# Kernel optimization log

Measured on AMD Instinct MI355X. Metric: run time of the kernel, lower is better.

The kernel has to match this reference:

```python
import jax, jax.numpy as jnp
import numpy as np

B, N, K = 8, 2048, 20  # clouds, points per cloud, knn


def _lin(k, i, o):
    kw, kb = jax.random.split(k)
    w = jax.random.normal(kw, (i, o), jnp.float32) / np.sqrt(i)
    b = jax.random.normal(kb, (o,), jnp.float32) * 0.01
    return w, b


def setup_inputs():
    key = jax.random.key(0)
    ks = jax.random.split(key, 9)
    pos = jax.random.normal(ks[0], (B * N, 3), jnp.float32)
    w11, b11 = _lin(ks[1], 3, 64)
    w12, b12 = _lin(ks[2], 64, 64)
    w13, b13 = _lin(ks[3], 64, 64)
    w21, b21 = _lin(ks[4], 192, 128)
    wh1, bh1 = _lin(ks[5], 128, 1024)
    wh2, bh2 = _lin(ks[6], 1024, 512)
    wh3, bh3 = _lin(ks[7], 512, 265)
    wh4, bh4 = _lin(ks[8], 265, 40)
    o, z = jnp.ones, jnp.zeros
    return dict(
        pos=pos,
        w11=w11, b11=b11, g11=o(64), be11=z(64),
        w12=w12, b12=b12, g12=o(64), be12=z(64),
        w13=w13, b13=b13, g13=o(64), be13=z(64),
        w21=w21, b21=b21, g21=o(128), be21=z(128),
        wh1=wh1, bh1=bh1, gh1=o(1024), beh1=z(1024),
        wh2=wh2, bh2=bh2, gh2=o(512), beh2=z(512),
        wh3=wh3, bh3=bh3, gh3=o(265), beh3=z(265),
        wh4=wh4, bh4=bh4,
    )


def _bn(x, g, b):
    # BatchNorm1d in training mode: stats over all leading dims, biased var.
    ax = tuple(range(x.ndim - 1))
    m = x.mean(ax)
    v = x.var(ax)
    return (x - m) * jax.lax.rsqrt(v + 1e-5) * g + b


def _forward(pos, w11, b11, g11, be11, w12, b12, g12, be12, w13, b13, g13, be13,
             w21, b21, g21, be21, wh1, bh1, gh1, beh1, wh2, bh2, gh2, beh2,
             wh3, bh3, gh3, beh3, wh4, bh4):
    p = pos.reshape(B, N, 3)
    # knn_graph per cloud, loop=False
    d2 = jnp.sum(p * p, -1)                                   # [B,N]
    dist = d2[:, :, None] + d2[:, None, :] - 2.0 * jnp.einsum('bnd,bmd->bnm', p, p)
    dist = dist + jnp.eye(N, dtype=pos.dtype) * 1e10          # exclude self
    _, idx = jax.lax.top_k(-dist, K)                          # [B,N,K]
    nb = jax.vmap(lambda a, i: a[i])(p, idx)                  # [B,N,K,3]
    rel = nb - p[:, :, None, :]                               # relative neighbor offsets
    # local PCA frame per point (V_t)
    cov = jnp.einsum('bnkd,bnke->bnde', rel, rel)             # [B,N,3,3]
    _, V = jnp.linalg.eigh(cov)                               # columns = principal dirs
    loc = jnp.einsum('bnkd,bnde->bnke', rel, V)               # rel pos in local frame
    # DD1: edge MLP (conv_p) + directional max pool (out_3d)
    h = _bn(jax.nn.relu(loc @ w11 + b11), g11, be11)
    h = _bn(jax.nn.relu(h @ w12 + b12), g12, be12)
    h = _bn(jax.nn.relu(h @ w13 + b13), g13, be13)            # [B,N,K,64]
    f3d = jnp.max(h[..., None] * loc[..., None, :], axis=2)   # [B,N,64,3]
    # DD2: gather neighbor 3d features (conv_fn), rotate into center frame, MLP, max pool
    fj = jax.vmap(lambda a, i: a[i])(f3d, idx)                # [B,N,K,64,3]
    fj_loc = jnp.einsum('bnkcd,bnde->bnkce', fj, V)
    h2 = _bn(jax.nn.relu(fj_loc.reshape(B, N, K, 192) @ w21 + b21), g21, be21)
    fdd2 = jnp.max(h2, axis=2).reshape(B * N, 128)
    # head
    y1 = (fdd2 @ wh1 + bh1).reshape(B, N, 1024).max(axis=1)
    y1 = _bn(jax.nn.relu(y1), gh1, beh1)
    y2 = _bn(jax.nn.relu(y1 @ wh2 + bh2), gh2, beh2)
    y3 = _bn(jax.nn.relu(y2 @ wh3 + bh3), gh3, beh3)
    return jax.nn.log_softmax(y3 @ wh4 + bh4, axis=1)         # [B,40]


def reference(pos, w11, b11, g11, be11, w12, b12, g12, be12, w13, b13, g13, be13,
              w21, b21, g21, be21, wh1, bh1, gh1, beh1, wh2, bh2, gh2, beh2,
              wh3, bh3, gh3, beh3, wh4, bh4):
    return _forward(pos, w11, b11, g11, be11, w12, b12, g12, be12, w13, b13, g13, be13,
                    w21, b21, g21, be21, wh1, bh1, gh1, beh1, wh2, bh2, gh2, beh2,
                    wh3, bh3, gh3, beh3, wh4, bh4)
```

## Files before the change

### kernel.cpp

```cpp
#include <hip/hip_runtime.h>


#define NEW_SLARTG 1

typedef unsigned short u16;
typedef unsigned int u32;
typedef unsigned long long u64;
typedef __attribute__((ext_vector_type(8))) short short8;
typedef __attribute__((ext_vector_type(4))) float f32x4;

#define BB 8
#define NNp 2048
#define KKn 20
#define NP 16384
#define EE 327680

__device__ __forceinline__ u32 fkey(float f) {
  u32 u = __float_as_uint(f);
  return (u & 0x80000000u) ? ~u : (u | 0x80000000u);
}
__device__ __forceinline__ float funkey(u32 k) {
  u32 u = (k & 0x80000000u) ? (k ^ 0x80000000u) : ~k;
  return __uint_as_float(u);
}
__device__ __forceinline__ float f_sign(float a, float b) {
  return (b >= 0.f) ? fabsf(a) : -fabsf(a);
}
__device__ __forceinline__ u16 f2bf(float f) {
  u32 u = __float_as_uint(f);
  u32 r = (u + 0x7fffu + ((u >> 16) & 1u)) >> 16;
  return (u16)r;
}

__device__ __forceinline__ u64 sxor64(u64 v, int m) {
  union { u64 q; u32 d[2]; } a; a.q = v;
  a.d[0] = __shfl_xor(a.d[0], m);
  a.d[1] = __shfl_xor(a.d[1], m);
  return a.q;
}
__device__ __forceinline__ u64 sidx64(u64 v, int src) {
  union { u64 q; u32 d[2]; } a; a.q = v;
  a.d[0] = __shfl(a.d[0], src);
  a.d[1] = __shfl(a.d[1], src);
  return a.q;
}
__device__ __forceinline__ void bsort64(u64& v, int lane) {
#pragma unroll
  for (int k = 2; k <= 64; k <<= 1) {
#pragma unroll
    for (int j = k >> 1; j > 0; j >>= 1) {
      u64 pv = sxor64(v, j);
      bool up = ((lane & k) == 0);
      bool lower = ((lane & j) == 0);
      bool keepmin = (lower == up);
      bool take = keepmin ? (pv < v) : (pv > v);
      v = take ? pv : v;
    }
  }
}

__device__ float slapy2_(float x, float y) {
#pragma clang fp contract(off)
  float xa = fabsf(x), ya = fabsf(y);
  float w = fmaxf(xa, ya), z = fminf(xa, ya);
  if (z == 0.f) return w;
  float t = z / w;
  return w * sqrtf(1.0f + t * t);
}

__device__ void slartg_(float f, float g, float& c, float& s, float& r) {
#pragma clang fp contract(off)
#if NEW_SLARTG
  const float safmin = 1.17549435e-38f;
  const float safmax = 8.50705917e+37f;
  const float rtmin = 1.08420217e-19f;
  const float rtmax = 6.52221171e+18f;
  float f1 = fabsf(f), g1 = fabsf(g);
  if (g == 0.f) { c = 1.f; s = 0.f; r = f; }
  else if (f == 0.f) { c = 0.f; s = (g >= 0.f) ? 1.f : -1.f; r = g1; }
  else {
    float d;
    if (f1 > rtmin && f1 < rtmax && g1 > rtmin && g1 < rtmax) {
      d = sqrtf(f * f + g * g);
      c = f1 / d;
      r = (f >= 0.f) ? d : -d;
    } else {
      float uu = fminf(safmax, fmaxf(safmin, fmaxf(f1, g1)));
      float fs = f / uu, gs = g / uu;
      d = sqrtf(fs * fs + gs * gs);
      c = fabsf(fs) / d;
      r = ((f >= 0.f) ? d : -d) * uu;
    }
    s = g / r;
  }
#else
  if (g == 0.f) { c = 1.f; s = 0.f; r = f; }
  else if (f == 0.f) { c = 0.f; s = 1.f; r = g; }
  else {
    float f1 = f, g1 = g;
    r = sqrtf(f1 * f1 + g1 * g1);
    c = f1 / r;
    s = g1 / r;
    if (fabsf(f) > fabsf(g) && c < 0.f) { c = -c; s = -s; r = -r; }
  }
#endif
}

__device__ void slaev2_(float a, float b, float c, float& rt1, float& rt2,
                        float& cs1, float& sn1) {
#pragma clang fp contract(off)
  float sm = a + c;
  float df = a - c;
  float adf = fabsf(df);
  float tb = b + b;
  float ab = fabsf(tb);
  float acmx, acmn;
  if (fabsf(a) > fabsf(c)) { acmx = a; acmn = c; } else { acmx = c; acmn = a; }
  float rt;
  if (adf > ab) { float t = ab / adf; rt = adf * sqrtf(1.f + t * t); }
  else if (adf < ab) { float t = adf / ab; rt = ab * sqrtf(1.f + t * t); }
  else { rt = ab * sqrtf(2.f); }
  int sgn1;
  if (sm < 0.f) {
    rt1 = 0.5f * (sm - rt); sgn1 = -1;
    rt2 = (acmx / rt1) * acmn - (b / rt1) * b;
  } else if (sm > 0.f) {
    rt1 = 0.5f * (sm + rt); sgn1 = 1;
    rt2 = (acmx / rt1) * acmn - (b / rt1) * b;
  } else {
    rt1 = 0.5f * rt; rt2 = -0.5f * rt; sgn1 = 1;
  }
  float cs; int sgn2;
  if (df >= 0.f) { cs = df + rt; sgn2 = 1; } else { cs = df - rt; sgn2 = -1; }
  float acs = fabsf(cs);
  if (acs > ab) {
    float ct = -tb / cs;
    sn1 = 1.f / sqrtf(1.f + ct * ct);
    cs1 = ct * sn1;
  } else {
    if (ab == 0.f) { cs1 = 1.f; sn1 = 0.f; }
    else {
      float tn = -cs / tb;
      cs1 = 1.f / sqrtf(1.f + tn * tn);
      sn1 = tn * cs1;
    }
  }
  if (sgn1 == sgn2) { float tn = cs1; cs1 = -sn1; sn1 = tn; }
}

__device__ void ssteqr3_(float* d, float* e, float z[3][3]) {
#pragma clang fp contract(off)
  const float eps = 5.9604645e-08f;
  const float eps2 = 3.5527137e-15f;
  const float safmin = 1.17549435e-38f;
  const int n = 3;
  const int nmaxit = 90;
  int jtot = 0;
  int l1 = 1;

  while (1) {
    if (l1 > n) break;
    if (l1 > 1) e[l1 - 2] = 0.f;
    int m = n;
    if (l1 <= n - 1) {
      for (int mm = l1; mm <= n - 1; ++mm) {
        float tst = fabsf(e[mm - 1]);
        if (tst == 0.f) { m = mm; break; }
        if (tst <= (sqrtf(fabsf(d[mm - 1])) * sqrtf(fabsf(d[mm]))) * eps) {
          e[mm - 1] = 0.f; m = mm; break;
        }
      }
    }
    int l = l1, lsv = l, lend = m, lendsv = lend;
    (void)lsv; (void)lendsv;
    l1 = m + 1;
    if (lend == l) continue;

    float anorm = 0.f;
    for (int i = l; i <= lend; ++i) anorm = fmaxf(anorm, fabsf(d[i - 1]));
    for (int i = l; i <= lend - 1; ++i) anorm = fmaxf(anorm, fabsf(e[i - 1]));
    if (anorm == 0.f) continue;

    if (fabsf(d[lend - 1]) < fabsf(d[l - 1])) { lend = lsv; l = lendsv; }

    if (lend > l) {
      while (1) {
        int m2 = lend;
        if (l != lend) {
          for (int mm = l; mm <= lend - 1; ++mm) {
            float tst = fabsf(e[mm - 1]); tst = tst * tst;
            if (tst <= (eps2 * fabsf(d[mm - 1])) * fabsf(d[mm]) + safmin) { m2 = mm; break; }
          }
        }
        if (m2 < lend) e[m2 - 1] = 0.f;
        float p = d[l - 1];
        if (m2 == l) {
          d[l - 1] = p; l += 1;
          if (l <= lend) continue;
          break;
        }
        if (m2 == l + 1) {
          float rt1, rt2, cc, ss;
          slaev2_(d[l - 1], e[l - 1], d[l], rt1, rt2, cc, ss);
          for (int i = 0; i < 3; ++i) {
            float temp = z[i][l];
            z[i][l] = cc * temp - ss * z[i][l - 1];
            z[i][l - 1] = ss * temp + cc * z[i][l - 1];
          }
          d[l - 1] = rt1; d[l] = rt2; e[l - 1] = 0.f;
          l += 2;
          if (l <= lend) continue;
          break;
        }
        if (jtot == nmaxit) break;
        jtot++;
        float g = (d[l] - p) / (2.f * e[l - 1]);
        float r = slapy2_(g, 1.f);
        g = d[m2 - 1] - p + (e[l - 1] / (g + f_sign(r, g)));
        float s = 1.f, c = 1.f;
        p = 0.f;
        float csv[2], snv[2];
        for (int i = m2 - 1; i >= l; --i) {
          float f = s * e[i - 1];
          float b = c * e[i - 1];
          slartg_(g, f, c, s, r);
          if (i != m2 - 1) e[i] = r;
          g = d[i] - p;
          r = (d[i - 1] - g) * s + (2.f * c) * b;
          p = s * r;
          d[i] = g + p;
          g = c * r - b;
          csv[i - l] = c; snv[i - l] = -s;
        }
        int cnt = m2 - l;
        for (int j = cnt; j >= 1; --j) {
          float cj = csv[j - 1], sj = snv[j - 1];
          int c0 = (l - 1) + (j - 1);
          for (int i = 0; i < 3; ++i) {
            float temp = z[i][c0 + 1];
            z[i][c0 + 1] = cj * temp - sj * z[i][c0];
            z[i][c0] = sj * temp + cj * z[i][c0];
          }
        }
        d[l - 1] = d[l - 1] - p;
        e[l - 1] = g;
      }
    } else {
      while (1) {
        int m2 = lend;
        if (l != lend) {
          for (int mm = l; mm >= lend + 1; --mm) {
            float tst = fabsf(e[mm - 2]); tst = tst * tst;
            if (tst <= (eps2 * fabsf(d[mm - 1])) * fabsf(d[mm - 2]) + safmin) { m2 = mm; break; }
          }
        }
        if (m2 > lend) e[m2 - 2] = 0.f;
        float p = d[l - 1];
        if (m2 == l) {
          d[l - 1] = p; l -= 1;
          if (l >= lend) continue;
          break;
        }
        if (m2 == l - 1) {
          float rt1, rt2, cc, ss;
          slaev2_(d[l - 2], e[l - 2], d[l - 1], rt1, rt2, cc, ss);
          for (int i = 0; i < 3; ++i) {
            float temp = z[i][l - 1];
            z[i][l - 1] = cc * temp - ss * z[i][l - 2];
            z[i][l - 2] = ss * temp + cc * z[i][l - 2];
          }
          d[l - 2] = rt1; d[l - 1] = rt2; e[l - 2] = 0.f;
          l -= 2;
          if (l >= lend) continue;
          break;
        }
        if (jtot == nmaxit) break;
        jtot++;
        float g = (d[l - 2] - p) / (2.f * e[l - 2]);
        float r = slapy2_(g, 1.f);
        g = d[m2 - 1] - p + (e[l - 2] / (g + f_sign(r, g)));
        float s = 1.f, c = 1.f;
        p = 0.f;
        float csv[2], snv[2];
        for (int i = m2; i <= l - 1; ++i) {
          float f = s * e[i - 1];
          float b = c * e[i - 1];
          slartg_(g, f, c, s, r);
          if (i != m2) e[i - 2] = r;
          g = d[i - 1] - p;
          r = (d[i] - g) * s + (2.f * c) * b;
          p = s * r;
          d[i - 1] = g + p;
          g = c * r - b;
          csv[i - m2] = c; snv[i - m2] = s;
        }
        int cnt = l - m2;
        for (int j = 1; j <= cnt; ++j) {
          float cj = csv[j - 1], sj = snv[j - 1];
          int c0 = (m2 - 1) + (j - 1);
          for (int i = 0; i < 3; ++i) {
            float temp = z[i][c0 + 1];
            z[i][c0 + 1] = cj * temp - sj * z[i][c0];
            z[i][c0] = sj * temp + cj * z[i][c0];
          }
        }
        d[l - 1] = d[l - 1] - p;
        e[l - 2] = g;
      }
    }
  }

  for (int ii = 2; ii <= n; ++ii) {
    int i = ii - 1, k = i;
    float p = d[i - 1];
    for (int j = ii; j <= n; ++j)
      if (d[j - 1] < p) { k = j; p = d[j - 1]; }
    if (k != i) {
      d[k - 1] = d[i - 1]; d[i - 1] = p;
      for (int r2 = 0; r2 < 3; ++r2) {
        float t = z[r2][i - 1]; z[r2][i - 1] = z[r2][k - 1]; z[r2][k - 1] = t;
      }
    }
  }
}

__device__ void eigh3_(float a00, float a10, float a11, float a20, float a21,
                       float a22, float V[3][3]) {
#pragma clang fp contract(off)
  float d0, d1, d2, e0, e1, tau1 = 0.f, v2 = 0.f;
  {
    float alpha = a10;
    float xnorm = fabsf(a20);
    if (xnorm == 0.f) {
      tau1 = 0.f; v2 = 0.f;
      e0 = alpha; d0 = a00; d1 = a11; d2 = a22; e1 = a21;
    } else {
      float beta = -f_sign(slapy2_(alpha, xnorm), alpha);
      tau1 = (beta - alpha) / beta;
      float inv = 1.0f / (alpha - beta);
      v2 = a20 * inv;
      float y0 = tau1 * a11;
      float y1v = tau1 * a21;
      float temp2 = a21 * v2;
      y0 = y0 + tau1 * temp2;
      y1v = y1v + (tau1 * v2) * a22;
      float dotyv = y0 * 1.f + y1v * v2;
      float al = (-0.5f * tau1) * dotyv;
      float w0 = y0 + al * 1.f;
      float w1 = y1v + al * v2;
      a11 = (a11 + 1.f * (-w0)) + w0 * (-1.f);
      a21 = (a21 + v2 * (-w0)) + w1 * (-1.f);
      a22 = (a22 + v2 * (-w1)) + w1 * (-v2);
      e0 = beta; d0 = a00; d1 = a11; d2 = a22; e1 = a21;
    }
  }
  float dd[3] = { d0, d1, d2 };
  float ee[2] = { e0, e1 };
  float z[3][3] = { {1.f,0.f,0.f},{0.f,1.f,0.f},{0.f,0.f,1.f} };
  ssteqr3_(dd, ee, z);
  if (tau1 != 0.f) {
    for (int j = 0; j < 3; ++j) {
      float wj = z[1][j] * 1.f + z[2][j] * v2;
      float temp = -tau1 * wj;
      z[1][j] = z[1][j] + 1.f * temp;
      z[2][j] = z[2][j] + v2 * temp;
    }
  }
  for (int r = 0; r < 3; ++r)
    for (int cix = 0; cix < 3; ++cix)
      V[r][cix] = z[r][cix];
}


__global__ void zero_kernel(double* sb, int nd, u32* p2, int n2) {
  int t = blockIdx.x * blockDim.x + threadIdx.x;
  if (t < nd) sb[t] = 0.0;
  if (t < n2) p2[t] = 0u;
}

__global__ __launch_bounds__(256) void knn_kernel(const float* __restrict__ pos,
                                                  int* __restrict__ idx) {
#pragma clang fp contract(off)
  __shared__ u64 cke[4][128];
  int w = threadIdx.x >> 6;
  int lane = threadIdx.x & 63;
  int wid = blockIdx.x * 4 + w;
  int b = wid >> 11;
  int n = wid & 2047;
  const float* pc = pos + (size_t)b * NNp * 3;
  float qx = pc[n * 3 + 0], qy = pc[n * 3 + 1], qz = pc[n * 3 + 2];
  float d2n = (qx * qx + qy * qy) + qz * qz;

  u32 kreg[32];
  u32 mk = 0xFFFFFFFFu;
#pragma unroll
  for (int t = 0; t < 32; ++t) {
    int m = lane + 64 * t;
    float x = pc[m * 3 + 0], y = pc[m * 3 + 1], zc = pc[m * 3 + 2];
    float d2m = (x * x + y * y) + zc * zc;
    float dot = (qx * x + qy * y) + qz * zc;
    float dist = (d2n + d2m) - 2.0f * dot;
    u32 key = fkey(dist);
    if (m == n) key = 0xFFFFFFFFu;
    kreg[t] = key;
    mk = key < mk ? key : mk;
  }
#pragma unroll
  for (int off = 32; off; off >>= 1) {
    u32 o = __shfl_xor(mk, off);
    mk = o < mk ? o : mk;
  }

  u32 lo_b = mk - 1u, hi_b = 0xFFFFFFFEu;
  int c_hi = 2047;
  float tf = funkey(mk) * 7.368f;
  u32 T = fkey(tf);
  if (T < mk) T = mk;
  if (T > 0xFFFFFFFEu) T = 0xFFFFFFFEu;
  for (int it = 0; it < 48; ++it) {
    int cnt = 0;
#pragma unroll
    for (int t = 0; t < 32; ++t) cnt += (kreg[t] <= T) ? 1 : 0;
#pragma unroll
    for (int off = 32; off; off >>= 1) cnt += __shfl_xor(cnt, off);
    if (cnt >= 20) {
      hi_b = T; c_hi = cnt;
      if (cnt <= 128) break;
    } else {
      lo_b = T;
    }
    if (hi_b <= lo_b + 1u) break;
    u32 Tn;
    if (it < 12) {
      float tfc = funkey(T);
      int cc = cnt < 1 ? 1 : cnt;
      float guess = tfc * __builtin_exp2f(0.66667f * __builtin_log2f(45.0f / (float)cc));
      Tn = fkey(guess);
      if (!(Tn > lo_b && Tn < hi_b)) Tn = lo_b + ((hi_b - lo_b) >> 1);
    } else {
      Tn = lo_b + ((hi_b - lo_b) >> 1);
    }
    T = Tn;
  }

  u64* ck = cke[w];
  u32 base = 0;
#pragma unroll
  for (int t = 0; t < 32; ++t) {
    bool pass = kreg[t] <= hi_b;
    u64 ball = __ballot(pass);
    if (pass) {
      u32 posn = base + (u32)__popcll(ball & ((1ull << lane) - 1ull));
      if (posn < 128u)
        ck[posn] = ((u64)kreg[t] << 32) | (u32)(lane + 64 * t);
    }
    base += (u32)__popcll(ball);
  }
  if (base > 128u) {
    base = 0;
#pragma unroll
    for (int t = 0; t < 32; ++t) {
      bool pass = kreg[t] <= lo_b;
      u64 ball = __ballot(pass);
      if (pass) {
        u32 posn = base + (u32)__popcll(ball & ((1ull << lane) - 1ull));
        ck[posn] = ((u64)kreg[t] << 32) | (u32)(lane + 64 * t);
      }
      base += (u32)__popcll(ball);
    }
#pragma unroll
    for (int t = 0; t < 32; ++t) {
      bool pass = (kreg[t] > lo_b) && (kreg[t] <= hi_b);
      u64 ball = __ballot(pass);
      if (pass) {
        u32 posn = base + (u32)__popcll(ball & ((1ull << lane) - 1ull));
        if (posn < 128u)
          ck[posn] = ((u64)kreg[t] << 32) | (u32)(lane + 64 * t);
      }
      base += (u32)__popcll(ball);
    }
  }
  u32 ctot = base < 128u ? base : 128u;

  u64 e0 = (lane < (int)ctot) ? ck[lane] : ~0ull;
  bsort64(e0, lane);
  if (ctot > 64u) {
    u64 e1 = (lane + 64 < (int)ctot) ? ck[lane + 64] : ~0ull;
    bsort64(e1, lane);
    u64 r = sidx64(e1, 63 - lane);
    u64 mn = r < e0 ? r : e0;
#pragma unroll
    for (int j = 32; j > 0; j >>= 1) {
      u64 pv = sxor64(mn, j);
      bool lower2 = ((lane & j) == 0);
      bool take = lower2 ? (pv < mn) : (pv > mn);
      mn = take ? pv : mn;
    }
    e0 = mn;
  }
  if (lane < 20)
    idx[(size_t)wid * 20 + lane] = (int)(u32)(e0 & 0xFFFFFFFFull);
}

__global__ __launch_bounds__(64) void prep_kernel(const float* __restrict__ pos,
                                                  const int* __restrict__ idx,
                                                  float* __restrict__ loc,
                                                  float* __restrict__ Vout) {
#pragma clang fp contract(off)
  int p = blockIdx.x * 64 + threadIdx.x;
  int b = p >> 11, n = p & 2047;
  const float* pc = pos + (size_t)b * NNp * 3;
  float qx = pc[n * 3 + 0], qy = pc[n * 3 + 1], qz = pc[n * 3 + 2];
  const int* ip = idx + (size_t)p * 20;
  float c00 = 0, c01 = 0, c02 = 0, c11 = 0, c12 = 0, c22 = 0;
  for (int k = 0; k < 20; ++k) {
    int j = ip[k];
    float rx = pc[j * 3 + 0] - qx, ry = pc[j * 3 + 1] - qy, rz = pc[j * 3 + 2] - qz;
    c00 += rx * rx; c01 += rx * ry; c02 += rx * rz;
    c11 += ry * ry; c12 += ry * rz; c22 += rz * rz;
  }
  float Vm[3][3];
  eigh3_(c00, c01, c11, c02, c12, c22, Vm);
  float* vp = Vout + (size_t)p * 9;
  for (int d = 0; d < 3; ++d)
    for (int e = 0; e < 3; ++e) vp[d * 3 + e] = Vm[d][e];
  for (int k = 0; k < 20; ++k) {
    int j = ip[k];
    float rx = pc[j * 3 + 0] - qx, ry = pc[j * 3 + 1] - qy, rz = pc[j * 3 + 2] - qz;
    float l0 = rx * Vm[0][0] + ry * Vm[1][0] + rz * Vm[2][0];
    float l1 = rx * Vm[0][1] + ry * Vm[1][1] + rz * Vm[2][1];
    float l2 = rx * Vm[0][2] + ry * Vm[1][2] + rz * Vm[2][2];
    size_t e = ((size_t)p * 20 + k) * 3;
    loc[e + 0] = l0; loc[e + 1] = l1; loc[e + 2] = l2;
  }
}

__global__ __launch_bounds__(256) void l1_kernel(const float* __restrict__ loc,
                                                 const float* __restrict__ W,
                                                 const float* __restrict__ bias,
                                                 float* __restrict__ h1,
                                                 double* __restrict__ sb) {
  __shared__ float sW[192];
  __shared__ float sB[64];
  __shared__ float red[512];
  int t = threadIdx.x;
  if (t < 192) sW[t] = W[t];
  if (t < 64) sB[t] = bias[t];
  __syncthreads();
  int w = t >> 6, c = t & 63;
  size_t e0 = (size_t)blockIdx.x * 256 + w * 64;
  float wc0 = sW[c], wc1 = sW[64 + c], wc2 = sW[128 + c], bc = sB[c];
  float s = 0.f, q = 0.f;
  for (int e = 0; e < 64; ++e) {
    float x0 = loc[(e0 + e) * 3 + 0];
    float x1 = loc[(e0 + e) * 3 + 1];
    float x2 = loc[(e0 + e) * 3 + 2];
    float z = fmaxf(bc + x0 * wc0 + x1 * wc1 + x2 * wc2, 0.f);
    h1[(e0 + e) * 64 + c] = z;
    s += z; q += z * z;
  }
  red[w * 64 + c] = s;
  red[256 + w * 64 + c] = q;
  __syncthreads();
  if (t < 64) {
    float S = red[t] + red[64 + t] + red[128 + t] + red[192 + t];
    float Q = red[256 + t] + red[320 + t] + red[384 + t] + red[448 + t];
    atomicAdd(&sb[((int)blockIdx.x & 63) * 128 + t], (double)S);
    atomicAdd(&sb[((int)blockIdx.x & 63) * 128 + 64 + t], (double)Q);
  }
}

__global__ void finalizeB_kernel(const double* __restrict__ sb,
                                 const float* __restrict__ g,
                                 const float* __restrict__ be,
                                 float* __restrict__ outp) {
  int c = threadIdx.x;
  if (c >= 64) return;
  double s = 0.0, q = 0.0;
  for (int buk = 0; buk < 64; ++buk) {
    s += sb[buk * 128 + c];
    q += sb[buk * 128 + 64 + c];
  }
  double m = s / (double)EE;
  double var = q / (double)EE - m * m;
  double inv = 1.0 / sqrt(var + 1e-5);
  double sc = (double)g[c] * inv;
  outp[c] = (float)sc;
  outp[64 + c] = (float)((double)be[c] - m * sc);
}

__global__ void finalize64_kernel(const double* __restrict__ s4b,
                                  const float* __restrict__ g,
                                  const float* __restrict__ be,
                                  float* __restrict__ outp) {
  int c = threadIdx.x;
  double s = 0.0, q = 0.0;
  for (int buk = 0; buk < 64; ++buk) {
    s += s4b[buk * 256 + c];
    q += s4b[buk * 256 + 128 + c];
  }
  double m = s / (double)EE;
  double var = q / (double)EE - m * m;
  double inv = 1.0 / sqrt(var + 1e-5);
  double sc = (double)g[c] * inv;
  outp[c] = (float)sc;
  outp[128 + c] = (float)((double)be[c] - m * sc);
}

__global__ __launch_bounds__(256) void l23_kernel(const float* __restrict__ hin,
                                                  const float* __restrict__ ss,
                                                  const float* __restrict__ W,
                                                  const float* __restrict__ bias,
                                                  float* __restrict__ hout,
                                                  double* __restrict__ sb) {
  __shared__ float xT[64 * 84];
  int t = threadIdx.x;
  size_t e0 = (size_t)blockIdx.x * 80;
  for (int v = t; v < 80 * 64; v += 256) {
    int el = v >> 6, c = v & 63;
    float val = hin[(e0 + el) * 64 + c];
    val = val * ss[c] + ss[64 + c];
    xT[c * 84 + el] = val;
  }
  __syncthreads();
  int og = t & 15, eg = t >> 4;
  int o0 = og * 4, eb = eg * 5;
  float acc[5][4];
#pragma unroll
  for (int a = 0; a < 5; ++a)
#pragma unroll
    for (int o = 0; o < 4; ++o) acc[a][o] = 0.f;
  for (int i = 0; i < 64; ++i) {
    float4 w4 = *(const float4*)&W[i * 64 + o0];
    float xx[5];
#pragma unroll
    for (int a = 0; a < 5; ++a) xx[a] = xT[i * 84 + eb + a];
#pragma unroll
    for (int a = 0; a < 5; ++a) {
      acc[a][0] += xx[a] * w4.x;
      acc[a][1] += xx[a] * w4.y;
      acc[a][2] += xx[a] * w4.z;
      acc[a][3] += xx[a] * w4.w;
    }
  }
  float4 b4 = *(const float4*)&bias[o0];
  float so0 = 0.f, so1 = 0.f, so2 = 0.f, so3 = 0.f;
  float qo0 = 0.f, qo1 = 0.f, qo2 = 0.f, qo3 = 0.f;
#pragma unroll
  for (int a = 0; a < 5; ++a) {
    size_t e = e0 + eb + a;
    float4 st;
    st.x = fmaxf(acc[a][0] + b4.x, 0.f);
    st.y = fmaxf(acc[a][1] + b4.y, 0.f);
    st.z = fmaxf(acc[a][2] + b4.z, 0.f);
    st.w = fmaxf(acc[a][3] + b4.w, 0.f);
    *(float4*)&hout[e * 64 + o0] = st;
    so0 += st.x; qo0 += st.x * st.x;
    so1 += st.y; qo1 += st.y * st.y;
    so2 += st.z; qo2 += st.z * st.z;
    so3 += st.w; qo3 += st.w * st.w;
  }
  __syncthreads();
  float* sred = xT;
  float* qred = xT + 1024;
  sred[(o0 + 0) * 16 + eg] = so0;
  sred[(o0 + 1) * 16 + eg] = so1;
  sred[(o0 + 2) * 16 + eg] = so2;
  sred[(o0 + 3) * 16 + eg] = so3;
  qred[(o0 + 0) * 16 + eg] = qo0;
  qred[(o0 + 1) * 16 + eg] = qo1;
  qred[(o0 + 2) * 16 + eg] = qo2;
  qred[(o0 + 3) * 16 + eg] = qo3;
  __syncthreads();
  if (t < 64) {
    float S = 0.f, Q = 0.f;
#pragma unroll
    for (int i = 0; i < 16; ++i) {
      S += sred[t * 16 + i];
      Q += qred[t * 16 + i];
    }
    atomicAdd(&sb[((int)blockIdx.x & 63) * 128 + t], (double)S);
    atomicAdd(&sb[((int)blockIdx.x & 63) * 128 + 64 + t], (double)Q);
  }
}

__global__ __launch_bounds__(256) void f3d_kernel(const float* __restrict__ h3,
                                                  const float* __restrict__ ss3,
                                                  const float* __restrict__ loc,
                                                  float* __restrict__ f3d) {
  int t = threadIdx.x;
  int p = blockIdx.x * 4 + (t >> 6);
  int c = t & 63;
  float sc = ss3[c], sh = ss3[64 + c];
  float m0 = -__builtin_inff(), m1 = m0, m2 = m0;
  size_t eb = (size_t)p * 20;
  for (int k = 0; k < 20; ++k) {
    size_t e = eb + k;
    float h = h3[e * 64 + c] * sc + sh;
    float l0 = loc[e * 3 + 0], l1 = loc[e * 3 + 1], l2 = loc[e * 3 + 2];
    m0 = fmaxf(m0, h * l0);
    m1 = fmaxf(m1, h * l1);
    m2 = fmaxf(m2, h * l2);
  }
  size_t o = (size_t)p * 192 + c * 3;
  f3d[o + 0] = m0; f3d[o + 1] = m1; f3d[o + 2] = m2;
}

__global__ __launch_bounds__(256) void wtcvt_kernel(const float* __restrict__ W,
                                                    u16* __restrict__ wt,
                                                    double* __restrict__ s4b) {
  int id = blockIdx.x * 256 + threadIdx.x;
  if (id < 192 * 128) {
    int n = id / 192, k = id - n * 192;
    wt[id] = f2bf(W[(size_t)k * 128 + n]);
  }
  if (id < 64 * 256) s4b[id] = 0.0;
}

__global__ __launch_bounds__(256) void dd2_kernel(const float* __restrict__ f3d,
                                                  const float* __restrict__ Vmat,
                                                  const int* __restrict__ idx,
                                                  const u16* __restrict__ wt,
                                                  const float* __restrict__ bias,
                                                  float* __restrict__ fdd2T,
                                                  double* __restrict__ s4b) {
  __shared__ u16 sX[80 * 200];
  __shared__ float sV[36];
  __shared__ int sJ[80];
  int t = threadIdx.x;
  int wk = (blockIdx.x & 7) * 512 + (blockIdx.x >> 3);
  int p0 = wk * 4;
  int bcl = p0 >> 11;
  int buk = ((int)blockIdx.x & 63) << 8;

  int w = t >> 6, l = t & 63;
  int lr = l & 15, lg = l >> 4;

  short8 breg[2][6];
#pragma unroll
  for (int nt = 0; nt < 2; ++nt)
#pragma unroll
    for (int s = 0; s < 6; ++s) {
      const int kk = (s / 3) * 96 + (s % 3) * 32 + lg * 8;
      breg[nt][s] = *(const short8*)&wt[(w * 32 + nt * 16 + lr) * 192 + kk];
    }

  if (t < 36) sV[t] = Vmat[(size_t)p0 * 9 + t];
  if (t < 80) sJ[t] = ((bcl << 11) + idx[(size_t)p0 * 20 + t]) * 192;
  __syncthreads();

  for (int v = t; v < 80 * 32; v += 256) {
    int el = v >> 5, c2 = v & 31;
    int pp = el / 20;
    const float* fp = f3d + (size_t)sJ[el] + 6 * c2;
    float f0 = fp[0], f1 = fp[1], f2 = fp[2];
    float f3 = fp[3], f4 = fp[4], f5 = fp[5];
    const float* Vp = &sV[pp * 9];
    float x0 = f0 * Vp[0] + f1 * Vp[3] + f2 * Vp[6];
    float x1 = f0 * Vp[1] + f1 * Vp[4] + f2 * Vp[7];
    float x2 = f0 * Vp[2] + f1 * Vp[5] + f2 * Vp[8];
    float y0 = f3 * Vp[0] + f4 * Vp[3] + f5 * Vp[6];
    float y1 = f3 * Vp[1] + f4 * Vp[4] + f5 * Vp[7];
    float y2 = f3 * Vp[2] + f4 * Vp[5] + f5 * Vp[8];
    u32* xp = (u32*)&sX[el * 200 + 6 * c2];
    xp[0] = (u32)f2bf(x0) | ((u32)f2bf(x1) << 16);
    xp[1] = (u32)f2bf(x2) | ((u32)f2bf(y0) << 16);
    xp[2] = (u32)f2bf(y1) | ((u32)f2bf(y2) << 16);
  }
  __syncthreads();

  f32x4 acc[5][2];
#pragma unroll
  for (int mt = 0; mt < 5; ++mt) {
    acc[mt][0] = (f32x4)(0.f);
    acc[mt][1] = (f32x4)(0.f);
  }

#pragma unroll
  for (int s = 0; s < 6; ++s) {
    const int kbase = (s / 3) * 96 + (s % 3) * 32 + lg * 8;
#pragma unroll
    for (int mt = 0; mt < 5; ++mt) {
      short8 a = *(const short8*)&sX[(mt * 16 + lr) * 200 + kbase];
      acc[mt][0] = __builtin_amdgcn_mfma_f32_16x16x32_bf16(a, breg[0][s], acc[mt][0], 0, 0, 0);
      acc[mt][1] = __builtin_amdgcn_mfma_f32_16x16x32_bf16(a, breg[1][s], acc[mt][1], 0, 0, 0);
    }
  }

#pragma unroll
  for (int nt = 0; nt < 2; ++nt) {
    int col = w * 32 + nt * 16 + lr;
    float bs = bias[col];
    float pm0 = 0.f, pm1 = 0.f, pm2 = 0.f, pm3 = 0.f;
    float s = 0.f, q = 0.f;
#pragma unroll
    for (int mt = 0; mt < 5; ++mt) {
#pragma unroll
      for (int r = 0; r < 4; ++r) {
        int edge = mt * 16 + lg * 4 + r;
        float z = fmaxf(acc[mt][nt][r] + bs, 0.f);
        pm0 = fmaxf(pm0, (edge < 20) ? z : 0.f);
        pm1 = fmaxf(pm1, (edge >= 20 && edge < 40) ? z : 0.f);
        pm2 = fmaxf(pm2, (edge >= 40 && edge < 60) ? z : 0.f);
        pm3 = fmaxf(pm3, (edge >= 60) ? z : 0.f);
        s += z; q += z * z;
      }
    }
#pragma unroll
    for (int off = 16; off < 64; off <<= 1) {
      pm0 = fmaxf(pm0, __shfl_xor(pm0, off));
      pm1 = fmaxf(pm1, __shfl_xor(pm1, off));
      pm2 = fmaxf(pm2, __shfl_xor(pm2, off));
      pm3 = fmaxf(pm3, __shfl_xor(pm3, off));
      s += __shfl_xor(s, off);
      q += __shfl_xor(q, off);
    }
    if (l < 16) {
      float4 pv;
      pv.x = pm0; pv.y = pm1; pv.z = pm2; pv.w = pm3;
      *(float4*)&fdd2T[(size_t)col * NP + p0] = pv;
      atomicAdd(&s4b[buk + col], (double)s);
      atomicAdd(&s4b[buk + 128 + col], (double)q);
    }
  }
}

__global__ __launch_bounds__(256) void y1_kernel(const float* __restrict__ fdd2T,
                                                 const float* __restrict__ ss4,
                                                 const float* __restrict__ wh1,
                                                 u32* __restrict__ y1key) {
  __shared__ float sX[64][128];
  __shared__ float sW[64][128];
  int t = threadIdx.x;
  int mtile = blockIdx.x & 127;
  int ntile = blockIdx.x >> 7;
  int cl = mtile >> 4;
  size_t pbase = (size_t)mtile * 128;
  int c0 = ntile * 128;
  int mg = t >> 4, ng = t & 15;

  float acc[8][8];
#pragma unroll
  for (int i = 0; i < 8; ++i)
#pragma unroll
    for (int j = 0; j < 8; ++j) acc[i][j] = 0.f;

  for (int ks = 0; ks < 2; ++ks) {
    int rr = t >> 5, mq = t & 31;
#pragma unroll
    for (int i = 0; i < 8; ++i) {
      int r = rr + i * 8;
      int k = ks * 64 + r;
      float4 x4 = *(const float4*)&fdd2T[(size_t)k * NP + pbase + mq * 4];
      float sc = ss4[k], sh = ss4[128 + k];
      float4 st;
      st.x = x4.x * sc + sh;
      st.y = x4.y * sc + sh;
      st.z = x4.z * sc + sh;
      st.w = x4.w * sc + sh;
      *(float4*)&sX[r][mq * 4] = st;
      float4 w4 = *(const float4*)&wh1[(size_t)k * 1024 + c0 + mq * 4];
      *(float4*)&sW[r][mq * 4] = w4;
    }
    __syncthreads();
#pragma unroll 8
    for (int kk = 0; kk < 64; ++kk) {
      float4 xa = *(const float4*)&sX[kk][mg * 4];
      float4 xb = *(const float4*)&sX[kk][64 + mg * 4];
      float4 wa = *(const float4*)&sW[kk][ng * 4];
      float4 wb = *(const float4*)&sW[kk][64 + ng * 4];
      float xr[8] = { xa.x, xa.y, xa.z, xa.w, xb.x, xb.y, xb.z, xb.w };
      float wc[8] = { wa.x, wa.y, wa.z, wa.w, wb.x, wb.y, wb.z, wb.w };
#pragma unroll
      for (int i = 0; i < 8; ++i)
#pragma unroll
        for (int j = 0; j < 8; ++j) acc[i][j] += xr[i] * wc[j];
    }
    __syncthreads();
  }

  float colmax[8];
#pragma unroll
  for (int j = 0; j < 8; ++j) {
    float v = acc[0][j];
#pragma unroll
    for (int i = 1; i < 8; ++i) v = fmaxf(v, acc[i][j]);
    colmax[j] = v;
  }
  float* red = &sX[0][0];
#pragma unroll
  for (int j = 0; j < 8; ++j) {
    int col = (j < 4) ? (ng * 4 + j) : (64 + ng * 4 + (j - 4));
    red[col * 16 + mg] = colmax[j];
  }
  __syncthreads();
  if (t < 128) {
    float m = red[t * 16];
#pragma unroll
    for (int i = 1; i < 16; ++i) m = fmaxf(m, red[t * 16 + i]);
    atomicMax(&y1key[(size_t)cl * 1024 + c0 + t], fkey(m));
  }
}

__global__ void y1bn_kernel(const u32* __restrict__ y1key,
                            const float* __restrict__ bh1,
                            const float* __restrict__ g,
                            const float* __restrict__ be,
                            float* __restrict__ y1n) {
  int c = blockIdx.x * 256 + threadIdx.x;
  if (c >= 1024) return;
  float bs = bh1[c];
  float v[8]; double s = 0.0;
#pragma unroll
  for (int b = 0; b < 8; ++b) {
    v[b] = fmaxf(funkey(y1key[b * 1024 + c]) + bs, 0.f);
    s += (double)v[b];
  }
  double m = s / 8.0, q = 0.0;
#pragma unroll
  for (int b = 0; b < 8; ++b) { double d = (double)v[b] - m; q += d * d; }
  q /= 8.0;
  double inv = 1.0 / sqrt(q + 1e-5);
  double sg = (double)g[c] * inv;
#pragma unroll
  for (int b = 0; b < 8; ++b)
    y1n[b * 1024 + c] = (float)(((double)v[b] - m) * sg + (double)be[c]);
}

__global__ __launch_bounds__(256) void hgemm_kernel(const float* __restrict__ yin,
                                                    const float* __restrict__ W,
                                                    float* __restrict__ part,
                                                    int INn, int OUTn, int notile) {
  __shared__ float sx[8 * 128];
  __shared__ float red[4][8][64];
  int t = threadIdx.x;
  int og = blockIdx.x % notile;
  int ks = blockIdx.x / notile;
  int KC = INn >> 3;
  int k0 = ks * KC;
  for (int v = t; v < 8 * KC; v += 256) {
    int b = v / KC, i = v - b * KC;
    sx[b * KC + i] = yin[(size_t)b * INn + k0 + i];
  }
  __syncthreads();
  int o = og * 64 + (t & 63);
  int kq = t >> 6;
  int sub = KC >> 2;
  float acc[8];
#pragma unroll
  for (int b = 0; b < 8; ++b) acc[b] = 0.f;
  if (o < OUTn) {
    for (int i = kq * sub; i < kq * sub + sub; ++i) {
      float w = W[(size_t)(k0 + i) * OUTn + o];
#pragma unroll
      for (int b = 0; b < 8; ++b) acc[b] += sx[b * KC + i] * w;
    }
  }
#pragma unroll
  for (int b = 0; b < 8; ++b) red[kq][b][t & 63] = acc[b];
  __syncthreads();
  if (kq == 0 && o < OUTn) {
#pragma unroll
    for (int b = 0; b < 8; ++b) {
      float s = ((red[0][b][t] + red[1][b][t]) + red[2][b][t]) + red[3][b][t];
      part[(size_t)(ks * 8 + b) * 512 + o] = s;
    }
  }
}

__global__ void hreduce_kernel(const float* __restrict__ part,
                               const float* __restrict__ bias,
                               const float* __restrict__ g,
                               const float* __restrict__ be,
                               float* __restrict__ yout, int OUTn) {
  int o = blockIdx.x * 256 + threadIdx.x;
  if (o >= OUTn) return;
  float bs = bias[o];
  float v[8]; double s = 0.0;
#pragma unroll
  for (int b = 0; b < 8; ++b) {
    float p = 0.f;
#pragma unroll
    for (int ks = 0; ks < 8; ++ks) p += part[(size_t)(ks * 8 + b) * 512 + o];
    v[b] = fmaxf(p + bs, 0.f);
    s += (double)v[b];
  }
  double m = s / 8.0, q = 0.0;
#pragma unroll
  for (int b = 0; b < 8; ++b) { double d = (double)v[b] - m; q += d * d; }
  q /= 8.0;
  double inv = 1.0 / sqrt(q + 1e-5);
  double sg = (double)g[o] * inv;
#pragma unroll
  for (int b = 0; b < 8; ++b)
    yout[(size_t)b * OUTn + o] = (float)(((double)v[b] - m) * sg + (double)be[o]);
}

__global__ __launch_bounds__(384) void logits_kernel(const float* __restrict__ y3n,
                                                     const float* __restrict__ W,
                                                     const float* __restrict__ bias,
                                                     float* __restrict__ out) {
  __shared__ float sy[8 * 265];
  __shared__ float slog[320];
  __shared__ float sm[8], sl[8];
  int t = threadIdx.x;
  for (int v = t; v < 8 * 265; v += 384) sy[v] = y3n[v];
  __syncthreads();
  if (t < 320) {
    int b = t / 40, o = t % 40;
    float acc = 0.f;
    for (int i = 0; i < 265; ++i) acc += sy[b * 265 + i] * W[i * 40 + o];
    slog[t] = acc + bias[o];
  }
  __syncthreads();
  if (t < 8) {
    float m = slog[t * 40];
    for (int o = 1; o < 40; ++o) m = fmaxf(m, slog[t * 40 + o]);
    float s = 0.f;
    for (int o = 0; o < 40; ++o) s += expf(slog[t * 40 + o] - m);
    sm[t] = m; sl[t] = logf(s);
  }
  __syncthreads();
  if (t < 320) {
    int b = t / 40;
    out[t] = slog[t] - sm[b] - sl[b];
  }
}

extern "C" void kernel_launch(void* const* d_in, const int* in_sizes, int n_in,
                              void* d_out, int out_size, void* d_ws, size_t ws_size,
                              hipStream_t stream) {
  (void)in_sizes; (void)n_in; (void)out_size; (void)ws_size;
  const float* pos  = (const float*)d_in[0];
  const float* w11  = (const float*)d_in[1];
  const float* b11  = (const float*)d_in[2];
  const float* g11  = (const float*)d_in[3];
  const float* be11 = (const float*)d_in[4];
  const float* w12  = (const float*)d_in[5];
  const float* b12  = (const float*)d_in[6];
  const float* g12  = (const float*)d_in[7];
  const float* be12 = (const float*)d_in[8];
  const float* w13  = (const float*)d_in[9];
  const float* b13  = (const float*)d_in[10];
  const float* g13  = (const float*)d_in[11];
  const float* be13 = (const float*)d_in[12];
  const float* w21  = (const float*)d_in[13];
  const float* b21  = (const float*)d_in[14];
  const float* g21  = (const float*)d_in[15];
  const float* be21 = (const float*)d_in[16];
  const float* wh1  = (const float*)d_in[17];
  const float* bh1  = (const float*)d_in[18];
  const float* gh1  = (const float*)d_in[19];
  const float* beh1 = (const float*)d_in[20];
  const float* wh2  = (const float*)d_in[21];
  const float* bh2  = (const float*)d_in[22];
  const float* gh2  = (const float*)d_in[23];
  const float* beh2 = (const float*)d_in[24];
  const float* wh3  = (const float*)d_in[25];
  const float* bh3  = (const float*)d_in[26];
  const float* gh3  = (const float*)d_in[27];
  const float* beh3 = (const float*)d_in[28];
  const float* wh4  = (const float*)d_in[29];
  const float* bh4  = (const float*)d_in[30];

  char* ws = (char*)d_ws;
  int*    idx   = (int*)(ws + 0);
  float*  loc   = (float*)(ws + 1310720);
  float*  V     = (float*)(ws + 5242880);
  float*  h     = (float*)(ws + 5832704);
  u16*    wt    = (u16*)(ws + 5832704);
  double* s4b   = (double*)(ws + 5898240);
  float*  hpart = (float*)(ws + 6881280);
  float*  f3d   = (float*)(ws + 89718784);
  double* sbkt  = (double*)(ws + 89718784);
  float*  fdd2T = (float*)(ws + 102301696);
  u32*    y1k   = (u32*)(ws + 110690304);
  float*  y1n   = (float*)(ws + 110723072);
  float*  y2n   = (float*)(ws + 110755840);
  float*  y3n   = (float*)(ws + 110772224);
  float*  param = (float*)(ws + 110785856);
  float*  out   = (float*)d_out;

  double* sbL1 = sbkt;
  double* sbL2 = sbkt + 8192;
  double* sbL3 = sbkt + 16384;

  zero_kernel<<<96, 256, 0, stream>>>(sbkt, 24576, y1k, 8192);
  knn_kernel<<<4096, 256, 0, stream>>>(pos, idx);
  prep_kernel<<<256, 64, 0, stream>>>(pos, idx, loc, V);

  l1_kernel<<<1280, 256, 0, stream>>>(loc, w11, b11, h, sbL1);
  finalizeB_kernel<<<1, 64, 0, stream>>>(sbL1, g11, be11, param);

  l23_kernel<<<4096, 256, 0, stream>>>(h, param, w12, b12, h, sbL2);
  finalizeB_kernel<<<1, 64, 0, stream>>>(sbL2, g12, be12, param + 128);

  l23_kernel<<<4096, 256, 0, stream>>>(h, param + 128, w13, b13, h, sbL3);
  finalizeB_kernel<<<1, 64, 0, stream>>>(sbL3, g13, be13, param + 256);

  f3d_kernel<<<4096, 256, 0, stream>>>(h, param + 256, loc, f3d);
  wtcvt_kernel<<<96, 256, 0, stream>>>(w21, wt, s4b);
  dd2_kernel<<<4096, 256, 0, stream>>>(f3d, V, idx, wt, b21, fdd2T, s4b);
  finalize64_kernel<<<1, 128, 0, stream>>>(s4b, g21, be21, param + 384);

  y1_kernel<<<1024, 256, 0, stream>>>(fdd2T, param + 384, wh1, y1k);
  y1bn_kernel<<<4, 256, 0, stream>>>(y1k, bh1, gh1, beh1, y1n);

  hgemm_kernel<<<64, 256, 0, stream>>>(y1n, wh2, hpart, 1024, 512, 8);
  hreduce_kernel<<<2, 256, 0, stream>>>(hpart, bh2, gh2, beh2, y2n, 512);
  hgemm_kernel<<<40, 256, 0, stream>>>(y2n, wh3, hpart, 512, 265, 5);
  hreduce_kernel<<<2, 256, 0, stream>>>(hpart, bh3, gh3, beh3, y3n, 265);
  logits_kernel<<<1, 384, 0, stream>>>(y3n, wh4, bh4, out);
}
```

Baseline: 386.8 us.

## Use split-bf16 MFMA for the 64x64 per-edge layers 2 and 3

Replaces the FP32 scalar FMA GEMM in the layer-2/3 kernel with bf16 MFMA instructions. Both activations and weights are split into hi+lo bf16 parts and three MFMAs per tile are accumulated to keep close to FP32 accuracy. A new prep kernel pre-splits and transposes the weights, tiles grow to 128 edges per block, and the BN statistics are reduced with wave shuffles instead of a shared-memory pass. The cost is extra conversion work and a small loss of precision from dropping the lo*lo term.

```diff
diff --git a/kernel.cpp b/kernel.cpp
--- a/kernel.cpp
+++ b/kernel.cpp
@@ -607,80 +607,117 @@
   outp[128 + c] = (float)((double)be[c] - m * sc);
 }
 
+__global__ __launch_bounds__(256) void wsplit_kernel(const float* __restrict__ w12,
+                                                     const float* __restrict__ w13,
+                                                     u16* __restrict__ wsp) {
+  int id = blockIdx.x * 256 + threadIdx.x;
+  if (id >= 8192) return;
+  int layer = id >> 12;
+  int nk = id & 4095;
+  int n = nk >> 6, k = nk & 63;
+  const float* W = layer ? w13 : w12;
+  float v = W[(size_t)k * 64 + n];
+  u16 hi = f2bf(v);
+  float rem = v - __uint_as_float(((u32)hi) << 16);
+  u16 lo = f2bf(rem);
+  wsp[layer * 8192 + n * 64 + k] = hi;
+  wsp[layer * 8192 + 4096 + n * 64 + k] = lo;
+}
+
 __global__ __launch_bounds__(256) void l23_kernel(const float* __restrict__ hin,
                                                   const float* __restrict__ ss,
-                                                  const float* __restrict__ W,
+                                                  const u16* __restrict__ whi,
+                                                  const u16* __restrict__ wlo,
                                                   const float* __restrict__ bias,
                                                   float* __restrict__ hout,
                                                   double* __restrict__ sb) {
-  __shared__ float xT[64 * 84];
+  __shared__ u16 sHI[128 * 72];
+  __shared__ u16 sLO[128 * 72];
   int t = threadIdx.x;
-  size_t e0 = (size_t)blockIdx.x * 80;
-  for (int v = t; v < 80 * 64; v += 256) {
-    int el = v >> 6, c = v & 63;
-    float val = hin[(e0 + el) * 64 + c];
-    val = val * ss[c] + ss[64 + c];
-    xT[c * 84 + el] = val;
+  size_t e0 = (size_t)blockIdx.x * 128;
+  int w = t >> 6, l = t & 63;
+  int lr = l & 15, lg = l >> 4;
+
+  short8 bhi[4][2], blo[4][2];
+#pragma unroll
+  for (int nt = 0; nt < 4; ++nt)
+#pragma unroll
+    for (int ks = 0; ks < 2; ++ks) {
+      int off = (nt * 16 + lr) * 64 + ks * 32 + lg * 8;
+      bhi[nt][ks] = *(const short8*)&whi[off];
+      blo[nt][ks] = *(const short8*)&wlo[off];
+    }
+
+  for (int v = t; v < 128 * 16; v += 256) {
+    int el = v >> 4, cq = v & 15;
+    float4 x4 = *(const float4*)&hin[(e0 + el) * 64 + cq * 4];
+    float4 sc4 = *(const float4*)&ss[cq * 4];
+    float4 sh4 = *(const float4*)&ss[64 + cq * 4];
+    float vv[4];
+    vv[0] = x4.x * sc4.x + sh4.x;
+    vv[1] = x4.y * sc4.y + sh4.y;
+    vv[2] = x4.z * sc4.z + sh4.z;
+    vv[3] = x4.w * sc4.w + sh4.w;
+    u16 hi[4], lo[4];
+#pragma unroll
+    for (int j = 0; j < 4; ++j) {
+      hi[j] = f2bf(vv[j]);
+      float rem = vv[j] - __uint_as_float(((u32)hi[j]) << 16);
+      lo[j] = f2bf(rem);
+    }
+    u32* ph = (u32*)&sHI[el * 72 + cq * 4];
+    ph[0] = (u32)hi[0] | ((u32)hi[1] << 16);
+    ph[1] = (u32)hi[2] | ((u32)hi[3] << 16);
+    u32* pl = (u32*)&sLO[el * 72 + cq * 4];
+    pl[0] = (u32)lo[0] | ((u32)lo[1] << 16);
+    pl[1] = (u32)lo[2] | ((u32)lo[3] << 16);
   }
   __syncthreads();
-  int og = t & 15, eg = t >> 4;
-  int o0 = og * 4, eb = eg * 5;
-  float acc[5][4];
-#pragma unroll
-  for (int a = 0; a < 5; ++a)
-#pragma unroll
-    for (int o = 0; o < 4; ++o) acc[a][o] = 0.f;
-  for (int i = 0; i < 64; ++i) {
-    float4 w4 = *(const float4*)&W[i * 64 + o0];
-    float xx[5];
-#pragma unroll
-    for (int a = 0; a < 5; ++a) xx[a] = xT[i * 84 + eb + a];
-#pragma unroll
-    for (int a = 0; a < 5; ++a) {
-      acc[a][0] += xx[a] * w4.x;
-      acc[a][1] += xx[a] * w4.y;
-      acc[a][2] += xx[a] * w4.z;
-      acc[a][3] += xx[a] * w4.w;
-    }
-  }
-  float4 b4 = *(const float4*)&bias[o0];
-  float so0 = 0.f, so1 = 0.f, so2 = 0.f, so3 = 0.f;
-  float qo0 = 0.f, qo1 = 0.f, qo2 = 0.f, qo3 = 0.f;
-#pragma unroll
-  for (int a = 0; a < 5; ++a) {
-    size_t e = e0 + eb + a;
-    float4 st;
-    st.x = fmaxf(acc[a][0] + b4.x, 0.f);
-    st.y = fmaxf(acc[a][1] + b4.y, 0.f);
-    st.z = fmaxf(acc[a][2] + b4.z, 0.f);
-    st.w = fmaxf(acc[a][3] + b4.w, 0.f);
-    *(float4*)&hout[e * 64 + o0] = st;
-    so0 += st.x; qo0 += st.x * st.x;
-    so1 += st.y; qo1 += st.y * st.y;
-    so2 += st.z; qo2 += st.z * st.z;
-    so3 += st.w; qo3 += st.w * st.w;
-  }
-  __syncthreads();
-  float* sred = xT;
-  float* qred = xT + 1024;
-  sred[(o0 + 0) * 16 + eg] = so0;
-  sred[(o0 + 1) * 16 + eg] = so1;
-  sred[(o0 + 2) * 16 + eg] = so2;
-  sred[(o0 + 3) * 16 + eg] = so3;
-  qred[(o0 + 0) * 16 + eg] = qo0;
-  qred[(o0 + 1) * 16 + eg] = qo1;
-  qred[(o0 + 2) * 16 + eg] = qo2;
-  qred[(o0 + 3) * 16 + eg] = qo3;
-  __syncthreads();
-  if (t < 64) {
-    float S = 0.f, Q = 0.f;
-#pragma unroll
-    for (int i = 0; i < 16; ++i) {
-      S += sred[t * 16 + i];
-      Q += qred[t * 16 + i];
-    }
-    atomicAdd(&sb[((int)blockIdx.x & 63) * 128 + t], (double)S);
-    atomicAdd(&sb[((int)blockIdx.x & 63) * 128 + 64 + t], (double)Q);
+
+  f32x4 acc[2][4];
+#pragma unroll
+  for (int mt = 0; mt < 2; ++mt)
+#pragma unroll
+    for (int nt = 0; nt < 4; ++nt) acc[mt][nt] = (f32x4)(0.f);
+
+#pragma unroll
+  for (int ks = 0; ks < 2; ++ks) {
+    const int kb = ks * 32 + lg * 8;
+#pragma unroll
+    for (int mt = 0; mt < 2; ++mt) {
+      int row = w * 32 + mt * 16 + lr;
+      short8 ah = *(const short8*)&sHI[row * 72 + kb];
+      short8 al = *(const short8*)&sLO[row * 72 + kb];
+#pragma unroll
+      for (int nt = 0; nt < 4; ++nt) {
+        acc[mt][nt] = __builtin_amdgcn_mfma_f32_16x16x32_bf16(ah, bhi[nt][ks], acc[mt][nt], 0, 0, 0);
+        acc[mt][nt] = __builtin_amdgcn_mfma_f32_16x16x32_bf16(al, bhi[nt][ks], acc[mt][nt], 0, 0, 0);
+        acc[mt][nt] = __builtin_amdgcn_mfma_f32_16x16x32_bf16(ah, blo[nt][ks], acc[mt][nt], 0, 0, 0);
+      }
+    }
+  }
+
+#pragma unroll
+  for (int nt = 0; nt < 4; ++nt) {
+    int o = nt * 16 + lr;
+    float bs = bias[o];
+    float s = 0.f, q = 0.f;
+#pragma unroll
+    for (int mt = 0; mt < 2; ++mt) {
+#pragma unroll
+      for (int r = 0; r < 4; ++r) {
+        float z = fmaxf(acc[mt][nt][r] + bs, 0.f);
+        size_t e = e0 + w * 32 + mt * 16 + lg * 4 + r;
+        hout[e * 64 + o] = z;
+        s += z; q += z * z;
+      }
+    }
+    s += __shfl_xor(s, 16); s += __shfl_xor(s, 32);
+    q += __shfl_xor(q, 16); q += __shfl_xor(q, 32);
+    if (l < 16) {
+      atomicAdd(&sb[((int)blockIdx.x & 63) * 128 + o], (double)s);
+      atomicAdd(&sb[((int)blockIdx.x & 63) * 128 + 64 + o], (double)q);
+    }
   }
 }
 
@@ -1073,6 +1110,7 @@
   float*  hpart = (float*)(ws + 6881280);
   float*  f3d   = (float*)(ws + 89718784);
   double* sbkt  = (double*)(ws + 89718784);
+  u16*    wsp   = (u16*)(ws + 89718784 + 196608);
   float*  fdd2T = (float*)(ws + 102301696);
   u32*    y1k   = (u32*)(ws + 110690304);
   float*  y1n   = (float*)(ws + 110723072);
@@ -1086,16 +1124,17 @@
   double* sbL3 = sbkt + 16384;
 
   zero_kernel<<<96, 256, 0, stream>>>(sbkt, 24576, y1k, 8192);
+  wsplit_kernel<<<32, 256, 0, stream>>>(w12, w13, wsp);
   knn_kernel<<<4096, 256, 0, stream>>>(pos, idx);
   prep_kernel<<<256, 64, 0, stream>>>(pos, idx, loc, V);
 
   l1_kernel<<<1280, 256, 0, stream>>>(loc, w11, b11, h, sbL1);
   finalizeB_kernel<<<1, 64, 0, stream>>>(sbL1, g11, be11, param);
 
-  l23_kernel<<<4096, 256, 0, stream>>>(h, param, w12, b12, h, sbL2);
+  l23_kernel<<<2560, 256, 0, stream>>>(h, param, wsp, wsp + 4096, b12, h, sbL2);
   finalizeB_kernel<<<1, 64, 0, stream>>>(sbL2, g12, be12, param + 128);
 
-  l23_kernel<<<4096, 256, 0, stream>>>(h, param + 128, w13, b13, h, sbL3);
+  l23_kernel<<<2560, 256, 0, stream>>>(h, param + 128, wsp + 8192, wsp + 12288, b13, h, sbL3);
   finalizeB_kernel<<<1, 64, 0, stream>>>(sbL3, g13, be13, param + 256);
 
   f3d_kernel<<<4096, 256, 0, stream>>>(h, param + 256, loc, f3d);
```

After: 370.0 us. 4.3% less time.
